# Kernel optimization log

Measured on AMD Instinct MI355X. Metric: run time of the kernel, lower is better.

## Reference

```python
import jax, jax.numpy as jnp
import numpy as np
from jax import lax

NUM_GRID = 16
THRESHOLD = 0.65
NUM_BG = 1
NUM_FG = 40
MAX_PTS = 42
T, C, H, W = 8, 4, 1024, 1024


def setup_inputs() -> dict:
    key = jax.random.key(0)
    k1, _ = jax.random.split(key)
    similarities = jax.random.uniform(k1, (T, C, H, W), dtype=jnp.float32)
    category_ids = jnp.arange(C, dtype=jnp.int32)
    original_sizes = jnp.full((T, 2), 2048, dtype=jnp.int32)
    return {"similarities": similarities, "category_ids": category_ids,
            "original_sizes": original_sizes}


def _process_one(sim, ori):
    """sim: [H, W] similarity map; ori: [2] original (H, W). Returns ([MAX_PTS,4], count)."""
    h, w = sim.shape
    dt = sim.dtype
    n = h * w
    flat = sim.reshape(-1)
    rows = jnp.arange(n, dtype=jnp.int32) // w   # y coords
    cols = jnp.arange(n, dtype=jnp.int32) % w    # x coords
    neg_inf = jnp.array(-jnp.inf, dtype=dt)

    # ---- foreground: threshold + per-grid-cell best (segment max) ----
    fg_mask = flat > THRESHOLD
    any_fg = jnp.any(fg_mask)
    # replicate original's naming: map_w, map_h = similarity_map.shape
    cell_w = h / NUM_GRID
    cell_h = w / NUM_GRID
    cxi = jnp.clip(jnp.floor(cols / cell_w).astype(jnp.int32), 0, NUM_GRID - 1)
    cyi = jnp.clip(jnp.floor(rows / cell_h).astype(jnp.int32), 0, NUM_GRID - 1)
    cid = cyi * NUM_GRID + cxi                        # [n] grid-cell id
    n_cells = NUM_GRID * NUM_GRID
    mscore = jnp.where(fg_mask, flat, neg_inf)
    cell_max = jax.ops.segment_max(mscore, cid, num_segments=n_cells)   # [n_cells]
    # first (lowest flat index) point achieving the cell max -> torch.topk tie-break
    is_best = fg_mask & (mscore == cell_max[cid])
    cand = jnp.where(is_best, jnp.arange(n, dtype=jnp.int32), n)
    cell_arg = jax.ops.segment_min(cand, cid, num_segments=n_cells)
    cell_valid = jnp.isfinite(cell_max)
    safe = jnp.where(cell_valid, cell_arg, 0)
    px = cols[safe].astype(dt)
    py = rows[safe].astype(dt)
    ps = flat[safe]
    # sort cells by score descending, keep top NUM_FG (filter_foreground_points)
    order = jnp.argsort(-jnp.where(cell_valid, ps, neg_inf))
    top = order[:NUM_FG]
    fg_x, fg_y, fg_s, fg_v = px[top], py[top], ps[top], cell_valid[top]
    n_valid = jnp.minimum(jnp.sum(cell_valid.astype(jnp.int32)), NUM_FG)
    # fallback when nothing exceeds threshold: global argmax (original uses // map_h == // W)
    gidx = jnp.argmax(flat)
    g_y = (gidx // w).astype(dt)
    g_x = (gidx % w).astype(dt)
    g_s = flat[gidx]
    slot0 = jnp.arange(NUM_FG) == 0
    fg_x = jnp.where(any_fg, fg_x, jnp.where(slot0, g_x, 0.0))
    fg_y = jnp.where(any_fg, fg_y, jnp.where(slot0, g_y, 0.0))
    fg_s = jnp.where(any_fg, fg_s, jnp.where(slot0, g_s, 0.0))
    fg_v = jnp.where(any_fg, fg_v, slot0)
    fg_count = jnp.where(any_fg, n_valid, 1)

    # ---- background: k smallest values over the map ----
    neg_vals, bidx = lax.top_k(-flat, NUM_BG)
    b_y = (bidx // w).astype(dt)
    b_x = (bidx % w).astype(dt)
    b_s = -neg_vals

    # ---- convert to original image coordinates ----
    sx = ori[1].astype(dt) / w
    sy = ori[0].astype(dt) / h
    fg_pts = jnp.stack([fg_x * sx, fg_y * sy, fg_s,
                        jnp.ones(NUM_FG, dtype=dt)], axis=-1)
    fg_pts = fg_pts * fg_v[:, None].astype(dt)        # zero out invalid rows
    bg_pts = jnp.stack([b_x * sx, b_y * sy, b_s,
                        jnp.zeros(NUM_BG, dtype=dt)], axis=-1)

    out = jnp.zeros((MAX_PTS, 4), dtype=dt)
    out = out.at[:NUM_FG].set(fg_pts)
    bg_rows = fg_count + jnp.arange(NUM_BG, dtype=jnp.int32)  # bg right after valid fg
    out = out.at[bg_rows].set(bg_pts)
    num = fg_count + NUM_BG
    return out, num


def _forward(similarities, original_sizes):
    per_cat = jax.vmap(_process_one, in_axes=(0, None))      # over C
    per_tgt = jax.vmap(per_cat, in_axes=(0, 0))              # over T
    points, nums = per_tgt(similarities, original_sizes)
    return points, nums.astype(jnp.int32)


def reference(similarities, category_ids, original_sizes):
    # category_ids is metadata (defines C); not used in the point math.
    return _forward(similarities, original_sizes)
```

## Files before the change

kernel.cpp:

```cpp
#include <hip/hip_runtime.h>
#include <math.h>

#define NUM_GRID 16
#define NCELLS   256
#define THRESH   0.65f
#define NUM_FG   40
#define NUM_BG   1
#define MAX_PTS  42
#define T_DIM    8
#define C_DIM    4
#define H_DIM    1024
#define W_DIM    1024
#define NMAPS    (T_DIM * C_DIM)
#define MAP_ELEMS (H_DIM * W_DIM)
#define CELL_DIM 64

__device__ inline void block_reduce_pair(float& v, int& i, bool is_max,
                                         float* sv, int* si, int tid) {
    sv[tid] = v; si[tid] = i;
    __syncthreads();
    for (int s = 128; s > 0; s >>= 1) {
        if (tid < s) {
            float v2 = sv[tid + s]; int i2 = si[tid + s];
            float v1 = sv[tid];     int i1 = si[tid];
            bool take = is_max ? (v2 > v1 || (v2 == v1 && i2 < i1))
                               : (v2 < v1 || (v2 == v1 && i2 < i1));
            if (take) { sv[tid] = v2; si[tid] = i2; }
        }
        __syncthreads();
    }
    v = sv[0]; i = si[0];
    __syncthreads();
}

__global__ __launch_bounds__(256)
void cell_stats_kernel(const float* __restrict__ sim,
                       float* __restrict__ fgmax_o, int* __restrict__ fgarg_o,
                       float* __restrict__ amax_o,  int* __restrict__ amaxarg_o,
                       float* __restrict__ amin_o,  int* __restrict__ aminarg_o) {
    const int b    = blockIdx.x;
    const int map  = b >> 8;
    const int cell = b & 255;
    const int cy   = cell >> 4;
    const int cx   = cell & 15;
    const int tid  = threadIdx.x;
    const int g    = tid & 15;
    const int rr   = tid >> 4;

    const float* base = sim + (size_t)map * MAP_ELEMS;

    float fgv = -INFINITY; int fgi = 0x7fffffff;
    float mxv = -INFINITY; int mxi = 0x7fffffff;
    float mnv =  INFINITY; int mni = 0x7fffffff;

    #pragma unroll
    for (int r = 0; r < 4; ++r) {
        const int row = cy * CELL_DIM + r * 16 + rr;
        const int col = cx * CELL_DIM + g * 4;
        const int idx = row * W_DIM + col;
        const float4 v4 = *reinterpret_cast<const float4*>(base + idx);
        const float vals[4] = {v4.x, v4.y, v4.z, v4.w};
        #pragma unroll
        for (int j = 0; j < 4; ++j) {
            const float v  = vals[j];
            const int   ix = idx + j;
            if (v > mxv) { mxv = v; mxi = ix; }
            if (v < mnv) { mnv = v; mni = ix; }
            if (v > THRESH && v > fgv) { fgv = v; fgi = ix; }
        }
    }

    __shared__ float sv[256];
    __shared__ int   si[256];

    block_reduce_pair(fgv, fgi, true,  sv, si, tid);
    block_reduce_pair(mxv, mxi, true,  sv, si, tid);
    block_reduce_pair(mnv, mni, false, sv, si, tid);

    if (tid == 0) {
        const int o = map * NCELLS + cell;
        fgmax_o[o]   = fgv;  fgarg_o[o]   = fgi;
        amax_o[o]    = mxv;  amaxarg_o[o] = mxi;
        amin_o[o]    = mnv;  aminarg_o[o] = mni;
    }
}

__global__ __launch_bounds__(256)
void select_kernel(const float* __restrict__ fgmax_i, const int* __restrict__ fgarg_i,
                   const float* __restrict__ amax_i,  const int* __restrict__ amaxarg_i,
                   const float* __restrict__ amin_i,  const int* __restrict__ aminarg_i,
                   const int* __restrict__ orig_sizes,
                   float* __restrict__ out_pts, float* __restrict__ out_nums) {
    const int m   = blockIdx.x;
    const int tid = threadIdx.x;
    const int t   = m >> 2;

    const float sx = (float)orig_sizes[t * 2 + 1] / (float)W_DIM;
    const float sy = (float)orig_sizes[t * 2 + 0] / (float)H_DIM;

    const int o = m * NCELLS + tid;
    const float fgv = fgmax_i[o];
    const int   fgi = fgarg_i[o];
    const bool  valid = (fgv > -INFINITY);

    __shared__ float skey[256];
    skey[tid] = fgv;

    __shared__ float sv[256];
    __shared__ int   si[256];

    float gv = amax_i[o]; int gi = amaxarg_i[o];
    block_reduce_pair(gv, gi, true, sv, si, tid);
    float bv = amin_i[o]; int bi = aminarg_i[o];
    block_reduce_pair(bv, bi, false, sv, si, tid);

    const int nvalid = __syncthreads_count(valid ? 1 : 0);
    const bool any_fg = (nvalid > 0);
    const int fg_count = any_fg ? (nvalid < NUM_FG ? nvalid : NUM_FG) : 1;

    int rank = 0;
    const float key = fgv;
    for (int j = 0; j < 256; ++j) {
        const float kj = skey[j];
        rank += (kj > key || (kj == key && j < tid)) ? 1 : 0;
    }

    __shared__ float outp[MAX_PTS * 4];
    if (tid < MAX_PTS * 4) outp[tid] = 0.0f;
    __syncthreads();

    if (any_fg && valid && rank < NUM_FG) {
        const int col = fgi & (W_DIM - 1);
        const int row = fgi >> 10;
        outp[rank * 4 + 0] = (float)col * sx;
        outp[rank * 4 + 1] = (float)row * sy;
        outp[rank * 4 + 2] = fgv;
        outp[rank * 4 + 3] = 1.0f;
    }
    if (!any_fg && tid == 0) {
        const int col = gi & (W_DIM - 1);
        const int row = gi >> 10;
        outp[0] = (float)col * sx;
        outp[1] = (float)row * sy;
        outp[2] = gv;
        outp[3] = 1.0f;
    }
    __syncthreads();

    if (tid == 0) {
        const int col = bi & (W_DIM - 1);
        const int row = bi >> 10;
        outp[fg_count * 4 + 0] = (float)col * sx;
        outp[fg_count * 4 + 1] = (float)row * sy;
        outp[fg_count * 4 + 2] = bv;
        outp[fg_count * 4 + 3] = 0.0f;
    }
    __syncthreads();

    if (tid < MAX_PTS * 4) out_pts[(size_t)m * (MAX_PTS * 4) + tid] = outp[tid];
    if (tid == 0) out_nums[m] = (float)(fg_count + NUM_BG);
}

extern "C" void kernel_launch(void* const* d_in, const int* in_sizes, int n_in,
                              void* d_out, int out_size, void* d_ws, size_t ws_size,
                              hipStream_t stream) {
    const float* sim        = (const float*)d_in[0];
    const int*   orig_sizes = (const int*)d_in[2];

    float* out = (float*)d_out;
    float* out_pts  = out;
    float* out_nums = out + (size_t)NMAPS * MAX_PTS * 4;

    const size_t NC = (size_t)NMAPS * NCELLS;
    char* ws = (char*)d_ws;
    float* fgmax_ws   = (float*)(ws + 0 * NC * 4);
    int*   fgarg_ws   = (int*)  (ws + 1 * NC * 4);
    float* amax_ws    = (float*)(ws + 2 * NC * 4);
    int*   amaxarg_ws = (int*)  (ws + 3 * NC * 4);
    float* amin_ws    = (float*)(ws + 4 * NC * 4);
    int*   aminarg_ws = (int*)  (ws + 5 * NC * 4);

    cell_stats_kernel<<<NMAPS * NCELLS, 256, 0, stream>>>(
        sim, fgmax_ws, fgarg_ws, amax_ws, amaxarg_ws, amin_ws, aminarg_ws);

    select_kernel<<<NMAPS, 256, 0, stream>>>(
        fgmax_ws, fgarg_ws, amax_ws, amaxarg_ws, amin_ws, aminarg_ws,
        orig_sizes, out_pts, out_nums);
}
```

Baseline: 202.7 us.

## Restructure cell stats into row-band blocks with shuffle reductions and derived fg max

Each block now scans a 32-row band of a whole map, with each thread walking a 4-wide column strip down the rows. Per-cell results come from 16-lane shuffle reductions instead of shared-memory tree reductions. The separate foreground max is dropped and derived in the select kernel as the cell max if it exceeds the threshold. Two half-cell partials per cell are merged in the select kernel. This removes the three block-wide syncthreads reductions per cell and cuts the grid from 8192 to 1024 blocks, at the cost of fewer, longer-running blocks.

```diff
diff --git a/kernel.cpp b/kernel.cpp
--- a/kernel.cpp
+++ b/kernel.cpp
@@ -14,6 +14,62 @@
 #define NMAPS    (T_DIM * C_DIM)
 #define MAP_ELEMS (H_DIM * W_DIM)
 #define CELL_DIM 64
+
+#define ROWS_PER_BLK 32
+#define BANDS_PER_MAP (H_DIM / ROWS_PER_BLK)
+#define NHALF 2
+
+__global__ __launch_bounds__(256)
+void cell_stats_kernel(const float* __restrict__ sim,
+                       float* __restrict__ amax_o, int* __restrict__ amaxarg_o,
+                       float* __restrict__ amin_o, int* __restrict__ aminarg_o) {
+    const int b    = blockIdx.x;
+    const int map  = b >> 5;
+    const int rb   = b & 31;
+    const int t    = threadIdx.x;
+    const int row0 = rb * ROWS_PER_BLK;
+
+    const float* __restrict__ p =
+        sim + (size_t)map * MAP_ELEMS + (size_t)row0 * W_DIM + (t << 2);
+    int idx = (row0 << 10) + (t << 2);
+
+    float mxv = -INFINITY; int mxi = 0;
+    float mnv =  INFINITY; int mni = 0;
+
+    #pragma unroll 8
+    for (int r = 0; r < ROWS_PER_BLK; ++r) {
+        const float4 v = *reinterpret_cast<const float4*>(p);
+        p += W_DIM;
+        if (v.x > mxv) { mxv = v.x; mxi = idx;     }
+        if (v.x < mnv) { mnv = v.x; mni = idx;     }
+        if (v.y > mxv) { mxv = v.y; mxi = idx + 1; }
+        if (v.y < mnv) { mnv = v.y; mni = idx + 1; }
+        if (v.z > mxv) { mxv = v.z; mxi = idx + 2; }
+        if (v.z < mnv) { mnv = v.z; mni = idx + 2; }
+        if (v.w > mxv) { mxv = v.w; mxi = idx + 3; }
+        if (v.w < mnv) { mnv = v.w; mni = idx + 3; }
+        idx += W_DIM;
+    }
+
+    #pragma unroll
+    for (int d = 1; d < 16; d <<= 1) {
+        const float v2 = __shfl_xor(mxv, d);
+        const int   i2 = __shfl_xor(mxi, d);
+        if (v2 > mxv || (v2 == mxv && i2 < mxi)) { mxv = v2; mxi = i2; }
+        const float u2 = __shfl_xor(mnv, d);
+        const int   j2 = __shfl_xor(mni, d);
+        if (u2 < mnv || (u2 == mnv && j2 < mni)) { mnv = u2; mni = j2; }
+    }
+
+    if ((t & 15) == 0) {
+        const int cx   = t >> 4;
+        const int cy   = rb >> 1;
+        const int half = rb & 1;
+        const int o = half * (NMAPS * NCELLS) + (map << 8) + (cy << 4) + cx;
+        amax_o[o] = mxv; amaxarg_o[o] = mxi;
+        amin_o[o] = mnv; aminarg_o[o] = mni;
+    }
+}
 
 __device__ inline void block_reduce_pair(float& v, int& i, bool is_max,
                                          float* sv, int* si, int tid) {
@@ -34,61 +90,8 @@
 }
 
 __global__ __launch_bounds__(256)
-void cell_stats_kernel(const float* __restrict__ sim,
-                       float* __restrict__ fgmax_o, int* __restrict__ fgarg_o,
-                       float* __restrict__ amax_o,  int* __restrict__ amaxarg_o,
-                       float* __restrict__ amin_o,  int* __restrict__ aminarg_o) {
-    const int b    = blockIdx.x;
-    const int map  = b >> 8;
-    const int cell = b & 255;
-    const int cy   = cell >> 4;
-    const int cx   = cell & 15;
-    const int tid  = threadIdx.x;
-    const int g    = tid & 15;
-    const int rr   = tid >> 4;
-
-    const float* base = sim + (size_t)map * MAP_ELEMS;
-
-    float fgv = -INFINITY; int fgi = 0x7fffffff;
-    float mxv = -INFINITY; int mxi = 0x7fffffff;
-    float mnv =  INFINITY; int mni = 0x7fffffff;
-
-    #pragma unroll
-    for (int r = 0; r < 4; ++r) {
-        const int row = cy * CELL_DIM + r * 16 + rr;
-        const int col = cx * CELL_DIM + g * 4;
-        const int idx = row * W_DIM + col;
-        const float4 v4 = *reinterpret_cast<const float4*>(base + idx);
-        const float vals[4] = {v4.x, v4.y, v4.z, v4.w};
-        #pragma unroll
-        for (int j = 0; j < 4; ++j) {
-            const float v  = vals[j];
-            const int   ix = idx + j;
-            if (v > mxv) { mxv = v; mxi = ix; }
-            if (v < mnv) { mnv = v; mni = ix; }
-            if (v > THRESH && v > fgv) { fgv = v; fgi = ix; }
-        }
-    }
-
-    __shared__ float sv[256];
-    __shared__ int   si[256];
-
-    block_reduce_pair(fgv, fgi, true,  sv, si, tid);
-    block_reduce_pair(mxv, mxi, true,  sv, si, tid);
-    block_reduce_pair(mnv, mni, false, sv, si, tid);
-
-    if (tid == 0) {
-        const int o = map * NCELLS + cell;
-        fgmax_o[o]   = fgv;  fgarg_o[o]   = fgi;
-        amax_o[o]    = mxv;  amaxarg_o[o] = mxi;
-        amin_o[o]    = mnv;  aminarg_o[o] = mni;
-    }
-}
-
-__global__ __launch_bounds__(256)
-void select_kernel(const float* __restrict__ fgmax_i, const int* __restrict__ fgarg_i,
-                   const float* __restrict__ amax_i,  const int* __restrict__ amaxarg_i,
-                   const float* __restrict__ amin_i,  const int* __restrict__ aminarg_i,
+void select_kernel(const float* __restrict__ amax_i, const int* __restrict__ amaxarg_i,
+                   const float* __restrict__ amin_i, const int* __restrict__ aminarg_i,
                    const int* __restrict__ orig_sizes,
                    float* __restrict__ out_pts, float* __restrict__ out_nums) {
     const int m   = blockIdx.x;
@@ -98,10 +101,18 @@
     const float sx = (float)orig_sizes[t * 2 + 1] / (float)W_DIM;
     const float sy = (float)orig_sizes[t * 2 + 0] / (float)H_DIM;
 
-    const int o = m * NCELLS + tid;
-    const float fgv = fgmax_i[o];
-    const int   fgi = fgarg_i[o];
-    const bool  valid = (fgv > -INFINITY);
+    const int o0 = m * NCELLS + tid;
+    const int o1 = NMAPS * NCELLS + o0;
+    float mxv = amax_i[o0]; int mxi = amaxarg_i[o0];
+    { const float v2 = amax_i[o1]; const int i2 = amaxarg_i[o1];
+      if (v2 > mxv || (v2 == mxv && i2 < mxi)) { mxv = v2; mxi = i2; } }
+    float mnv = amin_i[o0]; int mni = aminarg_i[o0];
+    { const float u2 = amin_i[o1]; const int j2 = aminarg_i[o1];
+      if (u2 < mnv || (u2 == mnv && j2 < mni)) { mnv = u2; mni = j2; } }
+
+    const bool  valid = (mxv > THRESH);
+    const float fgv   = valid ? mxv : -INFINITY;
+    const int   fgi   = mxi;
 
     __shared__ float skey[256];
     skey[tid] = fgv;
@@ -109,9 +120,9 @@
     __shared__ float sv[256];
     __shared__ int   si[256];
 
-    float gv = amax_i[o]; int gi = amaxarg_i[o];
+    float gv = mxv; int gi = mxi;
     block_reduce_pair(gv, gi, true, sv, si, tid);
-    float bv = amin_i[o]; int bi = aminarg_i[o];
+    float bv = mnv; int bi = mni;
     block_reduce_pair(bv, bi, false, sv, si, tid);
 
     const int nvalid = __syncthreads_count(valid ? 1 : 0);
@@ -171,19 +182,17 @@
     float* out_pts  = out;
     float* out_nums = out + (size_t)NMAPS * MAX_PTS * 4;
 
-    const size_t NC = (size_t)NMAPS * NCELLS;
+    const size_t NC = (size_t)NHALF * NMAPS * NCELLS;
     char* ws = (char*)d_ws;
-    float* fgmax_ws   = (float*)(ws + 0 * NC * 4);
-    int*   fgarg_ws   = (int*)  (ws + 1 * NC * 4);
-    float* amax_ws    = (float*)(ws + 2 * NC * 4);
-    int*   amaxarg_ws = (int*)  (ws + 3 * NC * 4);
-    float* amin_ws    = (float*)(ws + 4 * NC * 4);
-    int*   aminarg_ws = (int*)  (ws + 5 * NC * 4);
+    float* amax_ws    = (float*)(ws + 0 * NC * 4);
+    int*   amaxarg_ws = (int*)  (ws + 1 * NC * 4);
+    float* amin_ws    = (float*)(ws + 2 * NC * 4);
+    int*   aminarg_ws = (int*)  (ws + 3 * NC * 4);
 
-    cell_stats_kernel<<<NMAPS * NCELLS, 256, 0, stream>>>(
-        sim, fgmax_ws, fgarg_ws, amax_ws, amaxarg_ws, amin_ws, aminarg_ws);
+    cell_stats_kernel<<<NMAPS * BANDS_PER_MAP, 256, 0, stream>>>(
+        sim, amax_ws, amaxarg_ws, amin_ws, aminarg_ws);
 
     select_kernel<<<NMAPS, 256, 0, stream>>>(
-        fgmax_ws, fgarg_ws, amax_ws, amaxarg_ws, amin_ws, aminarg_ws,
+        amax_ws, amaxarg_ws, amin_ws, aminarg_ws,
         orig_sizes, out_pts, out_nums);
 }
```

Measured after the change: 202.7 us. No clear change (+0.0%).
